# Kernel optimization log

Measured on AMD Instinct MI355X. Metric: run time of the kernel, lower is better.

The kernel has to match this reference:

```python
import jax, jax.numpy as jnp
import numpy as np

D_MODEL = 1024
N_HEADS = 16
HEAD_DIM = D_MODEL // N_HEADS


def setup_inputs() -> dict:
    key = jax.random.key(0)
    ks = jax.random.split(key, 5)
    q = jax.random.normal(ks[0], (2, 2048, D_MODEL), dtype=jnp.float32)
    Wq = jax.random.normal(ks[1], (D_MODEL, D_MODEL), dtype=jnp.float32) * (1.0 / np.sqrt(D_MODEL))
    bq = jax.random.normal(ks[2], (D_MODEL,), dtype=jnp.float32) * 0.01
    Wo = jax.random.normal(ks[3], (D_MODEL, D_MODEL), dtype=jnp.float32) * (1.0 / np.sqrt(D_MODEL))
    bo = jax.random.normal(ks[4], (D_MODEL,), dtype=jnp.float32) * 0.01
    return {"q": q, "Wq": Wq, "bq": bq, "Wo": Wo, "bo": bo}


def reference(q, Wq, bq, Wo, bo):
    bs, S, dim = q.shape
    # NOTE: original module (bug-faithfully) projects Q, K and V all with WQ.
    proj = q @ Wq.T + bq  # [B, S, D]
    h = proj.reshape(bs, S, N_HEADS, HEAD_DIM).transpose(0, 2, 1, 3)  # [B, H, S, Dh]
    qh, kh, vh = h, h, h
    scale = HEAD_DIM ** -0.5
    attn = jnp.einsum('bhqd,bhkd->bhqk', qh, kh) * scale  # [B, H, S, S]
    scores = jax.nn.softmax(attn, axis=-1)
    # dropout is identity in inference mode
    vals = jnp.einsum('bhqk,bhkd->bhqd', scores, vh)  # [B, H, S, Dh]
    vals = vals.transpose(0, 2, 1, 3).reshape(bs, S, dim)
    return vals @ Wo.T + bo
```

## Files before the change

### kernel.cpp

```cpp
#include <hip/hip_runtime.h>

#define D_MODEL 1024
#define N_HEADS 16
#define HEAD_DIM 64
#define SEQ 2048
#define BATCH 2
#define M_TOTAL (BATCH*SEQ)

typedef __bf16 bf16;
typedef __bf16 bf16x8 __attribute__((ext_vector_type(8)));
typedef __bf16 bf16x4 __attribute__((ext_vector_type(4)));
typedef float  floatx4 __attribute__((ext_vector_type(4)));
typedef short  shortx4 __attribute__((ext_vector_type(4)));

#if __has_builtin(__builtin_amdgcn_exp2f)
#define EXP2F(x) __builtin_amdgcn_exp2f(x)
#else
#define EXP2F(x) __expf(0.69314718f * (x))
#endif

__device__ __forceinline__ floatx4 mfma16(bf16x4 a, bf16x4 b, floatx4 c) {
#if __has_builtin(__builtin_amdgcn_mfma_f32_16x16x16_bf16)
    return __builtin_amdgcn_mfma_f32_16x16x16_bf16(a, b, c, 0, 0, 0);
#else
    return __builtin_amdgcn_mfma_f32_16x16x16bf16_1k(
        __builtin_bit_cast(shortx4, a), __builtin_bit_cast(shortx4, b), c, 0, 0, 0);
#endif
}

__device__ __forceinline__ void gl2lds16(const bf16* g, bf16* l) {
    __builtin_amdgcn_global_load_lds(
        (const __attribute__((address_space(1))) unsigned int*)g,
        (__attribute__((address_space(3))) unsigned int*)l, 16, 0, 0);
}

#define WAITBAR(N) asm volatile("s_waitcnt vmcnt(" #N ")\n\ts_barrier" ::: "memory")

__global__ void cvt_all(const float* __restrict__ q, const float* __restrict__ Wq,
                        const float* __restrict__ Wo, bf16* __restrict__ qb,
                        bf16* __restrict__ wqb, bf16* __restrict__ wob) {
    int i = blockIdx.x * 256 + threadIdx.x;
    const float* src; bf16* dst; int off;
    if (i < 1048576)      { src = q;  dst = qb;  off = i; }
    else if (i < 1310720) { src = Wq; dst = wqb; off = i - 1048576; }
    else                  { src = Wo; dst = wob; off = i - 1310720; }
    float4 v = ((const float4*)src)[off];
    bf16x4 o;
    o[0] = (bf16)v.x; o[1] = (bf16)v.y; o[2] = (bf16)v.z; o[3] = (bf16)v.w;
    ((bf16x4*)dst)[off] = o;
}

template<int MODE>
__global__ __launch_bounds__(256, 4)
void gemm_bt_bias_t(const bf16* __restrict__ A, const bf16* __restrict__ B,
                    const float* __restrict__ bias, void* __restrict__ Cout,
                    bf16* __restrict__ Cout2, int M, int N, int K)
{
    __shared__ __align__(16) bf16 smem[18432];

    const int tid  = threadIdx.x;
    const int lane = tid & 63;
    const int wave = tid >> 6;
    const int quad = lane >> 4;
    const int l16  = lane & 15;
    const int lin  = blockIdx.x;
    const int m0   = ((lin & 7) * 4 + ((lin >> 3) & 3)) * 128;
    const int n0   = (lin >> 5) * 64;
    const int wm   = (wave >> 1) * 64;
    const int wn   = (wave & 1) * 32;

    floatx4 acc[4][2];
#pragma unroll
    for (int i = 0; i < 4; i++)
#pragma unroll
        for (int j = 0; j < 2; j++) acc[i][j] = (floatx4){0.f, 0.f, 0.f, 0.f};

    auto issue = [&](int base, int k0) {
#pragma unroll
        for (int it = 0; it < 2; it++) {
            int s = it * 256 + tid;
            int row = s >> 2, cl = (s & 3) ^ (row & 3);
            gl2lds16(A + (size_t)(m0 + row) * K + k0 + cl * 8, &smem[base + s * 8]);
        }
        {
            int s = tid;
            int row = s >> 2, cl = (s & 3) ^ (row & 3);
            gl2lds16(B + (size_t)(n0 + row) * K + k0 + cl * 8, &smem[base + 4096 + s * 8]);
        }
    };

    auto compute = [&](int base) {
        bf16x8 af[4], bfr[2];
#pragma unroll
        for (int i = 0; i < 4; i++) {
            int row = wm + i * 16 + l16;
            int phys = quad ^ (row & 3);
            af[i] = *(const bf16x8*)&smem[base + row * 32 + phys * 8];
        }
#pragma unroll
        for (int j = 0; j < 2; j++) {
            int row = wn + j * 16 + l16;
            int phys = quad ^ (row & 3);
            bfr[j] = *(const bf16x8*)&smem[base + 4096 + row * 32 + phys * 8];
        }
#pragma unroll
        for (int i = 0; i < 4; i++)
#pragma unroll
            for (int j = 0; j < 2; j++)
                acc[i][j] = __builtin_amdgcn_mfma_f32_16x16x32_bf16(
                    af[i], bfr[j], acc[i][j], 0, 0, 0);
    };

    const int NT = K >> 5;
    issue(0, 0);
    issue(6144, 32);
    for (int t = 0; t < NT - 1; ++t) {
        WAITBAR(3);
        if (t + 2 < NT) issue(((t + 2) % 3) * 6144, (t + 2) << 5);
        compute((t % 3) * 6144);
    }
    WAITBAR(0);
    compute(((NT - 1) % 3) * 6144);

    if constexpr (MODE == 0) {
        float* C = (float*)Cout;
#pragma unroll
        for (int j = 0; j < 2; j++) {
            int col  = n0 + wn + j * 16 + l16;
            float bv = bias[col];
#pragma unroll
            for (int i = 0; i < 4; i++) {
                int rbase = m0 + wm + i * 16 + quad * 4;
#pragma unroll
                for (int r = 0; r < 4; r++)
                    C[(size_t)(rbase + r) * N + col] = acc[i][j][r] + bv;
            }
        }
    } else {
        bf16* Cb = (bf16*)Cout;
        const int h  = n0 >> 6;
        const int b  = m0 >> 11;
        bf16x4 tile[4][2];
#pragma unroll
        for (int j = 0; j < 2; j++) {
            int dL   = wn + j * 16 + l16;
            float bv = bias[n0 + dL];
#pragma unroll
            for (int i = 0; i < 4; i++) {
                int sl = wm + i * 16 + quad * 4;
                int s0 = (m0 & 2047) + sl;
#pragma unroll
                for (int r = 0; r < 4; r++) {
                    float v = acc[i][j][r] + bv;
                    tile[i][j][r] = (bf16)v;
                    Cb[(((size_t)(b * N_HEADS + h) * SEQ + (s0 + r)) << 6) + dL] = (bf16)v;
                }
            }
        }
        __syncthreads();
#pragma unroll
        for (int j = 0; j < 2; j++) {
            int dL = wn + j * 16 + l16;
#pragma unroll
            for (int i = 0; i < 4; i++) {
                int sl = wm + i * 16 + quad * 4;
                *(bf16x4*)&smem[dL * 128 + (((sl >> 3) ^ (dL & 15)) * 8) + (sl & 7)] =
                    tile[i][j];
            }
        }
        __syncthreads();
        {
            int dL    = tid >> 2;
            int sbase = m0 & 2047;
            bf16* dstrow = Cout2 + ((size_t)(b * N_HEADS + h) * 64 + dL) * SEQ + sbase;
#pragma unroll
            for (int cc = 0; cc < 4; cc++) {
                int c    = (tid & 3) * 4 + cc;
                int phys = c ^ (dL & 15);
                *(bf16x8*)(dstrow + c * 8) = *(const bf16x8*)&smem[dL * 128 + phys * 8];
            }
        }
    }
}

__global__ __launch_bounds__(256, 3)
void flash_attn(const bf16* __restrict__ projbf, const bf16* __restrict__ projT,
                bf16* __restrict__ vals)
{
    __shared__ __align__(16) bf16 Ks[3][64 * 64];
    __shared__ __align__(16) bf16 Vt[3][64 * 64];

    const int tid  = threadIdx.x;
    const int lane = tid & 63;
    const int wave = tid >> 6;
    const int quad = lane >> 4;
    const int l16  = lane & 15;
    const int lin  = blockIdx.x;
    const int bh   = (lin & 7) * 4 + (lin >> 7);
    const int q0   = ((lin >> 3) & 15) * 128;
    const bf16* hK  = projbf + (size_t)bh * SEQ * 64;
    const bf16* hVt = projT  + (size_t)bh * 64 * SEQ;
    const int wq0  = wave * 32;

    bf16x8 qf[2][2];
#pragma unroll
    for (int nbi = 0; nbi < 2; nbi++)
#pragma unroll
        for (int ks = 0; ks < 2; ks++) {
            bf16x8 v = *(const bf16x8*)(hK + (size_t)(q0 + wq0 + nbi * 16 + l16) * 64
                                        + ks * 32 + quad * 8);
#pragma unroll
            for (int e = 0; e < 8; e++)
                v[e] = (bf16)((float)v[e] * 0.18033688f);
            qf[nbi][ks] = v;
        }
    asm volatile("s_waitcnt vmcnt(0)" ::: "memory");

    bf16x4 ones;
#pragma unroll
    for (int e = 0; e < 4; e++) ones[e] = (bf16)1.0f;

    floatx4 oacc[4][2];
#pragma unroll
    for (int mb = 0; mb < 4; mb++)
#pragma unroll
        for (int nbi = 0; nbi < 2; nbi++) oacc[mb][nbi] = (floatx4){0.f, 0.f, 0.f, 0.f};
    floatx4 lacc[2];
#pragma unroll
    for (int nbi = 0; nbi < 2; nbi++) lacc[nbi] = (floatx4){0.f, 0.f, 0.f, 0.f};

    auto issue = [&](int buf, int k0) {
#pragma unroll
        for (int it = 0; it < 2; it++) {
            int s = it * 256 + tid;
            int row = s >> 3, cl = (s & 7) ^ (row & 7);
            gl2lds16(hK + (size_t)(k0 + row) * 64 + cl * 8, &Ks[buf][s * 8]);
        }
#pragma unroll
        for (int it = 0; it < 2; it++) {
            int s = it * 256 + tid;
            int row = s >> 3, cl = (s & 7) ^ (row & 7);
            gl2lds16(hVt + (size_t)row * SEQ + k0 + cl * 8, &Vt[buf][s * 8]);
        }
    };

    auto compute = [&](int buf) {
#pragma unroll
        for (int kc = 0; kc < 4; kc++) {
            int krow = kc * 16 + l16;
            bf16x8 kf0 = *(const bf16x8*)&Ks[buf][krow * 64 + ((quad ^ (krow & 7)) * 8)];
            bf16x8 kf1 = *(const bf16x8*)&Ks[buf][krow * 64 + (((4 + quad) ^ (krow & 7)) * 8)];
            bf16x4 p4[2];
#pragma unroll
            for (int nbi = 0; nbi < 2; nbi++) {
                floatx4 s = __builtin_amdgcn_mfma_f32_16x16x32_bf16(
                    kf0, qf[nbi][0], (floatx4){0.f, 0.f, 0.f, 0.f}, 0, 0, 0);
                s = __builtin_amdgcn_mfma_f32_16x16x32_bf16(
                    kf1, qf[nbi][1], s, 0, 0, 0);
#pragma unroll
                for (int r = 0; r < 4; r++)
                    p4[nbi][r] = (bf16)EXP2F(s[r]);
            }
            __builtin_amdgcn_s_setprio(1);
#pragma unroll
            for (int nbi = 0; nbi < 2; nbi++)
                lacc[nbi] = mfma16(ones, p4[nbi], lacc[nbi]);
#pragma unroll
            for (int mb = 0; mb < 4; mb++) {
                int vrow = mb * 16 + l16;
                int c    = kc * 2 + (quad >> 1);
                bf16x4 vf = *(const bf16x4*)&Vt[buf][vrow * 64
                                + ((c ^ (vrow & 7)) * 8) + (quad & 1) * 4];
#pragma unroll
                for (int nbi = 0; nbi < 2; nbi++)
                    oacc[mb][nbi] = mfma16(vf, p4[nbi], oacc[mb][nbi]);
            }
            __builtin_amdgcn_s_setprio(0);
        }
    };

    issue(0, 0);
    issue(1, 64);
    for (int t = 0; t < 31; ++t) {
        WAITBAR(4);
        if (t < 30) issue((t + 2) % 3, (t + 2) * 64);
        compute(t % 3);
    }
    WAITBAR(0);
    compute(1);

    const int b = bh >> 4, h = bh & 15;
#pragma unroll
    for (int nbi = 0; nbi < 2; nbi++) {
        float rinv = 1.0f / lacc[nbi][0];
        int q = q0 + wq0 + nbi * 16 + l16;
#pragma unroll
        for (int mb = 0; mb < 4; mb++) {
            bf16x4 o4;
#pragma unroll
            for (int r = 0; r < 4; r++) o4[r] = (bf16)(oacc[mb][nbi][r] * rinv);
            *(bf16x4*)&vals[((size_t)b * SEQ + q) * D_MODEL + h * 64 + mb * 16 + quad * 4] = o4;
        }
    }
}

extern "C" void kernel_launch(void* const* d_in, const int* in_sizes, int n_in,
                              void* d_out, int out_size, void* d_ws, size_t ws_size,
                              hipStream_t stream)
{
    const float* q  = (const float*)d_in[0];
    const float* Wq = (const float*)d_in[1];
    const float* bq = (const float*)d_in[2];
    const float* Wo = (const float*)d_in[3];
    const float* bo = (const float*)d_in[4];
    float* out = (float*)d_out;

    char* ws = (char*)d_ws;
    bf16* qbf    = (bf16*)(ws);
    bf16* Wqbf   = (bf16*)(ws + (size_t)( 8 << 20));
    bf16* Wobf   = (bf16*)(ws + (size_t)(10 << 20));
    bf16* projbf = (bf16*)(ws + (size_t)(12 << 20));
    bf16* projT  = (bf16*)(ws + (size_t)(20 << 20));
    bf16* valsb  = (bf16*)(ws + (size_t)(28 << 20));

    cvt_all<<<6144, 256, 0, stream>>>(q, Wq, Wo, qbf, Wqbf, Wobf);

    gemm_bt_bias_t<1><<<512, 256, 0, stream>>>(qbf, Wqbf, bq, (void*)projbf,
                                               projT, M_TOTAL, D_MODEL, D_MODEL);

    flash_attn<<<512, 256, 0, stream>>>(projbf, projT, valsb);

    gemm_bt_bias_t<0><<<512, 256, 0, stream>>>(valsb, Wobf, bo, (void*)out,
                                               nullptr, M_TOTAL, D_MODEL, D_MODEL);
}
```

Measured before the change: 166.8 us.

## Fuse fp32-to-bf16 conversion into GEMM loads and drop the separate convert kernel

Removes the standalone cvt_all kernel. Both GEMMs now read fp32 inputs and weights straight from global memory into registers, convert them to bf16, and write them into swizzled LDS with a register-staged double buffer. The K tile grows from 32 to 64, launch bounds drop to 2 blocks per CU, and the async global-to-LDS loads are replaced with register staging and __syncthreads. It also drops the setprio hints in the attention kernel. The aim is to save the extra kernel launch and the bf16 round trip through memory, at the cost of re-reading and re-converting fp32 weights in every GEMM block, doubling global traffic for B, and lowering occupancy.

```diff
diff --git a/kernel.cpp b/kernel.cpp
--- a/kernel.cpp
+++ b/kernel.cpp
@@ -36,27 +36,16 @@
 
 #define WAITBAR(N) asm volatile("s_waitcnt vmcnt(" #N ")\n\ts_barrier" ::: "memory")
 
-__global__ void cvt_all(const float* __restrict__ q, const float* __restrict__ Wq,
-                        const float* __restrict__ Wo, bf16* __restrict__ qb,
-                        bf16* __restrict__ wqb, bf16* __restrict__ wob) {
-    int i = blockIdx.x * 256 + threadIdx.x;
-    const float* src; bf16* dst; int off;
-    if (i < 1048576)      { src = q;  dst = qb;  off = i; }
-    else if (i < 1310720) { src = Wq; dst = wqb; off = i - 1048576; }
-    else                  { src = Wo; dst = wob; off = i - 1310720; }
-    float4 v = ((const float4*)src)[off];
-    bf16x4 o;
-    o[0] = (bf16)v.x; o[1] = (bf16)v.y; o[2] = (bf16)v.z; o[3] = (bf16)v.w;
-    ((bf16x4*)dst)[off] = o;
-}
-
 template<int MODE>
-__global__ __launch_bounds__(256, 4)
-void gemm_bt_bias_t(const bf16* __restrict__ A, const bf16* __restrict__ B,
+__global__ __launch_bounds__(256, 2)
+void gemm_bt_bias_t(const void* __restrict__ Ap, const float* __restrict__ B,
                     const float* __restrict__ bias, void* __restrict__ Cout,
                     bf16* __restrict__ Cout2, int M, int N, int K)
 {
-    __shared__ __align__(16) bf16 smem[18432];
+    __shared__ __align__(16) bf16 smem[24576];
+
+    const float* Af = (const float*)Ap;
+    const bf16*  Ab = (const bf16*)Ap;
 
     const int tid  = threadIdx.x;
     const int lane = tid & 63;
@@ -75,52 +64,95 @@
 #pragma unroll
         for (int j = 0; j < 2; j++) acc[i][j] = (floatx4){0.f, 0.f, 0.f, 0.f};
 
-    auto issue = [&](int base, int k0) {
-#pragma unroll
-        for (int it = 0; it < 2; it++) {
-            int s = it * 256 + tid;
-            int row = s >> 2, cl = (s & 3) ^ (row & 3);
-            gl2lds16(A + (size_t)(m0 + row) * K + k0 + cl * 8, &smem[base + s * 8]);
-        }
-        {
-            int s = tid;
-            int row = s >> 2, cl = (s & 3) ^ (row & 3);
-            gl2lds16(B + (size_t)(n0 + row) * K + k0 + cl * 8, &smem[base + 4096 + s * 8]);
+    float4 areg[8];
+    bf16x8 areg16[4];
+    float4 breg[4];
+
+    auto loadT = [&](int k0) {
+        if constexpr (MODE == 1) {
+#pragma unroll
+            for (int i = 0; i < 8; i++) {
+                int f = i * 256 + tid, row = f >> 4, c4 = f & 15;
+                areg[i] = *(const float4*)&Af[(size_t)(m0 + row) * K + k0 + c4 * 4];
+            }
+        } else {
+#pragma unroll
+            for (int i = 0; i < 4; i++) {
+                int s = i * 256 + tid, row = s >> 3, c = s & 7;
+                areg16[i] = *(const bf16x8*)&Ab[(size_t)(m0 + row) * K + k0 + c * 8];
+            }
+        }
+#pragma unroll
+        for (int i = 0; i < 4; i++) {
+            int f = i * 256 + tid, row = f >> 4, c4 = f & 15;
+            breg[i] = *(const float4*)&B[(size_t)(n0 + row) * K + k0 + c4 * 4];
+        }
+    };
+
+    auto writeT = [&](int base) {
+        if constexpr (MODE == 1) {
+#pragma unroll
+            for (int i = 0; i < 8; i++) {
+                int f = i * 256 + tid, row = f >> 4, c4 = f & 15;
+                bf16x4 w;
+                w[0] = (bf16)areg[i].x; w[1] = (bf16)areg[i].y;
+                w[2] = (bf16)areg[i].z; w[3] = (bf16)areg[i].w;
+                *(bf16x4*)&smem[base + row * 64 + (((c4 >> 1) ^ (row & 7)) * 8)
+                                + (c4 & 1) * 4] = w;
+            }
+        } else {
+#pragma unroll
+            for (int i = 0; i < 4; i++) {
+                int s = i * 256 + tid, row = s >> 3, c = s & 7;
+                *(bf16x8*)&smem[base + row * 64 + ((c ^ (row & 7)) * 8)] = areg16[i];
+            }
+        }
+#pragma unroll
+        for (int i = 0; i < 4; i++) {
+            int f = i * 256 + tid, row = f >> 4, c4 = f & 15;
+            bf16x4 w;
+            w[0] = (bf16)breg[i].x; w[1] = (bf16)breg[i].y;
+            w[2] = (bf16)breg[i].z; w[3] = (bf16)breg[i].w;
+            *(bf16x4*)&smem[base + 8192 + row * 64 + (((c4 >> 1) ^ (row & 7)) * 8)
+                            + (c4 & 1) * 4] = w;
         }
     };
 
     auto compute = [&](int base) {
-        bf16x8 af[4], bfr[2];
-#pragma unroll
-        for (int i = 0; i < 4; i++) {
-            int row = wm + i * 16 + l16;
-            int phys = quad ^ (row & 3);
-            af[i] = *(const bf16x8*)&smem[base + row * 32 + phys * 8];
-        }
-#pragma unroll
-        for (int j = 0; j < 2; j++) {
-            int row = wn + j * 16 + l16;
-            int phys = quad ^ (row & 3);
-            bfr[j] = *(const bf16x8*)&smem[base + 4096 + row * 32 + phys * 8];
-        }
-#pragma unroll
-        for (int i = 0; i < 4; i++)
-#pragma unroll
-            for (int j = 0; j < 2; j++)
-                acc[i][j] = __builtin_amdgcn_mfma_f32_16x16x32_bf16(
-                    af[i], bfr[j], acc[i][j], 0, 0, 0);
-    };
-
-    const int NT = K >> 5;
-    issue(0, 0);
-    issue(6144, 32);
-    for (int t = 0; t < NT - 1; ++t) {
-        WAITBAR(3);
-        if (t + 2 < NT) issue(((t + 2) % 3) * 6144, (t + 2) << 5);
-        compute((t % 3) * 6144);
+#pragma unroll
+        for (int ks = 0; ks < 2; ks++) {
+            bf16x8 af[4], bfr[2];
+#pragma unroll
+            for (int i = 0; i < 4; i++) {
+                int row = wm + i * 16 + l16;
+                int phys = (ks * 4 + quad) ^ (row & 7);
+                af[i] = *(const bf16x8*)&smem[base + row * 64 + phys * 8];
+            }
+#pragma unroll
+            for (int j = 0; j < 2; j++) {
+                int row = wn + j * 16 + l16;
+                int phys = (ks * 4 + quad) ^ (row & 7);
+                bfr[j] = *(const bf16x8*)&smem[base + 8192 + row * 64 + phys * 8];
+            }
+#pragma unroll
+            for (int i = 0; i < 4; i++)
+#pragma unroll
+                for (int j = 0; j < 2; j++)
+                    acc[i][j] = __builtin_amdgcn_mfma_f32_16x16x32_bf16(
+                        af[i], bfr[j], acc[i][j], 0, 0, 0);
+        }
+    };
+
+    const int NT = K >> 6;
+    loadT(0);
+    writeT(0);
+    loadT(64);
+    for (int t = 0; t < NT; ++t) {
+        __syncthreads();
+        if (t + 1 < NT) writeT(((t + 1) & 1) * 12288);
+        if (t + 2 < NT) loadT((t + 2) << 6);
+        compute((t & 1) * 12288);
     }
-    WAITBAR(0);
-    compute(((NT - 1) % 3) * 6144);
 
     if constexpr (MODE == 0) {
         float* C = (float*)Cout;
@@ -261,7 +293,6 @@
                 for (int r = 0; r < 4; r++)
                     p4[nbi][r] = (bf16)EXP2F(s[r]);
             }
-            __builtin_amdgcn_s_setprio(1);
 #pragma unroll
             for (int nbi = 0; nbi < 2; nbi++)
                 lacc[nbi] = mfma16(ones, p4[nbi], lacc[nbi]);
@@ -275,7 +306,6 @@
                 for (int nbi = 0; nbi < 2; nbi++)
                     oacc[mb][nbi] = mfma16(vf, p4[nbi], oacc[mb][nbi]);
             }
-            __builtin_amdgcn_s_setprio(0);
         }
     };
 
@@ -316,20 +346,15 @@
     float* out = (float*)d_out;
 
     char* ws = (char*)d_ws;
-    bf16* qbf    = (bf16*)(ws);
-    bf16* Wqbf   = (bf16*)(ws + (size_t)( 8 << 20));
-    bf16* Wobf   = (bf16*)(ws + (size_t)(10 << 20));
-    bf16* projbf = (bf16*)(ws + (size_t)(12 << 20));
-    bf16* projT  = (bf16*)(ws + (size_t)(20 << 20));
-    bf16* valsb  = (bf16*)(ws + (size_t)(28 << 20));
-
-    cvt_all<<<6144, 256, 0, stream>>>(q, Wq, Wo, qbf, Wqbf, Wobf);
-
-    gemm_bt_bias_t<1><<<512, 256, 0, stream>>>(qbf, Wqbf, bq, (void*)projbf,
+    bf16* projbf = (bf16*)(ws);
+    bf16* projT  = (bf16*)(ws + (size_t)( 8 << 20));
+    bf16* valsb  = (bf16*)(ws + (size_t)(16 << 20));
+
+    gemm_bt_bias_t<1><<<512, 256, 0, stream>>>(q, Wq, bq, (void*)projbf,
                                                projT, M_TOTAL, D_MODEL, D_MODEL);
 
     flash_attn<<<512, 256, 0, stream>>>(projbf, projT, valsb);
 
-    gemm_bt_bias_t<0><<<512, 256, 0, stream>>>(valsb, Wobf, bo, (void*)out,
+    gemm_bt_bias_t<0><<<512, 256, 0, stream>>>(valsb, Wo, bo, (void*)out,
                                                nullptr, M_TOTAL, D_MODEL, D_MODEL);
 }
```

Measured after the change: 168.1 us. No clear change (+0.8%).

## Load GEMM fragments directly from global into registers, drop LDS staging

Applied to the files above, without the earlier changes.

Replaces the triple-buffered LDS pipeline in the projection GEMM with direct global-to-register fragment loads, double-buffered in registers, and fixes K at 1024 via a hard-coded 16-step loop. Occupancy target drops to 2 blocks per SM to make room for the extra registers. Removing the LDS copies and barriers is meant to cut synchronisation overhead, but each wave now reloads shared A/B tiles from global/L2 with no reuse across waves. Separately, the setprio hints around the attention MFMA section are removed.

```diff
diff --git a/kernel.cpp b/kernel.cpp
--- a/kernel.cpp
+++ b/kernel.cpp
@@ -51,12 +51,12 @@
 }
 
 template<int MODE>
-__global__ __launch_bounds__(256, 4)
+__global__ __launch_bounds__(256, 2)
 void gemm_bt_bias_t(const bf16* __restrict__ A, const bf16* __restrict__ B,
                     const float* __restrict__ bias, void* __restrict__ Cout,
                     bf16* __restrict__ Cout2, int M, int N, int K)
 {
-    __shared__ __align__(16) bf16 smem[18432];
+    __shared__ __align__(16) bf16 smem[8192];
 
     const int tid  = threadIdx.x;
     const int lane = tid & 63;
@@ -75,52 +75,58 @@
 #pragma unroll
         for (int j = 0; j < 2; j++) acc[i][j] = (floatx4){0.f, 0.f, 0.f, 0.f};
 
-    auto issue = [&](int base, int k0) {
-#pragma unroll
-        for (int it = 0; it < 2; it++) {
-            int s = it * 256 + tid;
-            int row = s >> 2, cl = (s & 3) ^ (row & 3);
-            gl2lds16(A + (size_t)(m0 + row) * K + k0 + cl * 8, &smem[base + s * 8]);
-        }
-        {
-            int s = tid;
-            int row = s >> 2, cl = (s & 3) ^ (row & 3);
-            gl2lds16(B + (size_t)(n0 + row) * K + k0 + cl * 8, &smem[base + 4096 + s * 8]);
-        }
-    };
-
-    auto compute = [&](int base) {
-        bf16x8 af[4], bfr[2];
-#pragma unroll
-        for (int i = 0; i < 4; i++) {
-            int row = wm + i * 16 + l16;
-            int phys = quad ^ (row & 3);
-            af[i] = *(const bf16x8*)&smem[base + row * 32 + phys * 8];
-        }
-#pragma unroll
-        for (int j = 0; j < 2; j++) {
-            int row = wn + j * 16 + l16;
-            int phys = quad ^ (row & 3);
-            bfr[j] = *(const bf16x8*)&smem[base + 4096 + row * 32 + phys * 8];
-        }
-#pragma unroll
-        for (int i = 0; i < 4; i++)
-#pragma unroll
-            for (int j = 0; j < 2; j++)
-                acc[i][j] = __builtin_amdgcn_mfma_f32_16x16x32_bf16(
-                    af[i], bfr[j], acc[i][j], 0, 0, 0);
-    };
-
-    const int NT = K >> 5;
-    issue(0, 0);
-    issue(6144, 32);
-    for (int t = 0; t < NT - 1; ++t) {
-        WAITBAR(3);
-        if (t + 2 < NT) issue(((t + 2) % 3) * 6144, (t + 2) << 5);
-        compute((t % 3) * 6144);
-    }
-    WAITBAR(0);
-    compute(((NT - 1) % 3) * 6144);
+    const bf16* pA[4];
+    const bf16* pB[2];
+#pragma unroll
+    for (int i = 0; i < 4; i++)
+        pA[i] = A + (size_t)(m0 + wm + i * 16 + l16) * K + quad * 8;
+#pragma unroll
+    for (int j = 0; j < 2; j++)
+        pB[j] = B + (size_t)(n0 + wn + j * 16 + l16) * K + quad * 8;
+
+    bf16x8 afX[4][2], bfX[2][2], afY[4][2], bfY[2][2];
+
+#define LDSET(af_, bf_, kk)                                                  \
+    {                                                                        \
+        _Pragma("unroll")                                                    \
+        for (int i = 0; i < 4; i++) {                                        \
+            _Pragma("unroll")                                                \
+            for (int ks = 0; ks < 2; ks++)                                   \
+                af_[i][ks] = *(const bf16x8*)(pA[i] + (kk) + ks * 32);       \
+        }                                                                    \
+        _Pragma("unroll")                                                    \
+        for (int j = 0; j < 2; j++) {                                        \
+            _Pragma("unroll")                                                \
+            for (int ks = 0; ks < 2; ks++)                                   \
+                bf_[j][ks] = *(const bf16x8*)(pB[j] + (kk) + ks * 32);       \
+        }                                                                    \
+    }
+
+#define MFMASET(af_, bf_)                                                    \
+    {                                                                        \
+        _Pragma("unroll")                                                    \
+        for (int ks = 0; ks < 2; ks++) {                                     \
+            _Pragma("unroll")                                                \
+            for (int i = 0; i < 4; i++) {                                    \
+                _Pragma("unroll")                                            \
+                for (int j = 0; j < 2; j++)                                  \
+                    acc[i][j] = __builtin_amdgcn_mfma_f32_16x16x32_bf16(     \
+                        af_[i][ks], bf_[j][ks], acc[i][j], 0, 0, 0);         \
+            }                                                                \
+        }                                                                    \
+    }
+
+    LDSET(afX, bfX, 0);
+#pragma unroll
+    for (int tt = 0; tt < 8; tt++) {
+        const int t0 = tt * 2;
+        if (t0 + 1 < 16) LDSET(afY, bfY, (t0 + 1) * 64);
+        MFMASET(afX, bfX);
+        if (t0 + 2 < 16) LDSET(afX, bfX, (t0 + 2) * 64);
+        MFMASET(afY, bfY);
+    }
+#undef LDSET
+#undef MFMASET
 
     if constexpr (MODE == 0) {
         float* C = (float*)Cout;
@@ -261,7 +267,6 @@
                 for (int r = 0; r < 4; r++)
                     p4[nbi][r] = (bf16)EXP2F(s[r]);
             }
-            __builtin_amdgcn_s_setprio(1);
 #pragma unroll
             for (int nbi = 0; nbi < 2; nbi++)
                 lacc[nbi] = mfma16(ones, p4[nbi], lacc[nbi]);
@@ -275,7 +280,6 @@
                 for (int nbi = 0; nbi < 2; nbi++)
                     oacc[mb][nbi] = mfma16(vf, p4[nbi], oacc[mb][nbi]);
             }
-            __builtin_amdgcn_s_setprio(0);
         }
     };
 
```

Result: slower. 230.0 us (+37.8%).
